# Kernel tuning notes

Hardware: AMD Instinct MI355X
Metric: run time of the kernel (lower is better)

Reference implementation:

```python
import jax, jax.numpy as jnp
import numpy as np

N = 100000      # nodes
E = 1600000     # edges
B = 64          # graphs in batch
V = 10000       # input_dim (embedding vocab)
EMB = 256       # emb_dim
HID = 64        # hidden_dim
OUT = 32        # output_dim


def setup_inputs() -> dict:
    key = jax.random.key(0)
    ks = jax.random.split(key, 12)
    state = jax.random.randint(ks[0], (B, 2), 0, V, dtype=jnp.int32)
    x = jax.random.randint(ks[1], (N,), 0, V, dtype=jnp.int32)
    edge_index = jax.random.randint(ks[2], (2, E), 0, N, dtype=jnp.int32)
    edge_weight = jnp.ones((E,), jnp.float32)
    # contiguous graph assignment (every graph non-empty)
    batch = jnp.minimum(jnp.arange(N, dtype=jnp.int32) // (N // B), B - 1)

    def lin(k, fin, fout):
        return jax.random.normal(k, (fin, fout), jnp.float32) / np.sqrt(fin).astype(np.float32)

    return {
        "state": state, "x": x, "edge_index": edge_index,
        "edge_weight": edge_weight, "batch": batch,
        "emb_table": jax.random.normal(ks[3], (V, EMB), jnp.float32),
        "W1": lin(ks[4], EMB, HID), "b1": jnp.zeros((HID,), jnp.float32),
        "W2": lin(ks[5], HID, HID), "b2": jnp.zeros((HID,), jnp.float32),
        "Wfc": lin(ks[6], HID, EMB), "bfc": jnp.zeros((EMB,), jnp.float32),
        "Wfc1": lin(ks[7], 3 * EMB, HID), "bfc1": jnp.zeros((HID,), jnp.float32),
        "Wfc2": lin(ks[8], HID, HID), "bfc2": jnp.zeros((HID,), jnp.float32),
        "Wfc3": lin(ks[9], HID, OUT), "bfc3": jnp.zeros((OUT,), jnp.float32),
    }


def gcn_conv(h, src, dst, ew, W, b):
    # PyG GCNConv: linear (no bias) -> sym-normalized aggregation w/ self loops -> + bias
    hw = h @ W                                           # [N, F_out]
    deg = jax.ops.segment_sum(ew, dst, num_segments=N) + 1.0  # +1 for self loop
    dinv = jax.lax.rsqrt(deg)                            # deg >= 1 always
    norm = dinv[src] * ew * dinv[dst]                    # [E]
    agg = jax.ops.segment_sum(norm[:, None] * hw[src], dst, num_segments=N)
    agg = agg + (dinv * dinv)[:, None] * hw              # self-loop contribution
    return agg + b


def reference(state, x, edge_index, edge_weight, batch, emb_table,
              W1, b1, W2, b2, Wfc, bfc, Wfc1, bfc1, Wfc2, bfc2, Wfc3, bfc3):
    src, dst = edge_index[0], edge_index[1]
    h = emb_table[x]                                     # [N, EMB]
    h = jax.nn.relu(gcn_conv(h, src, dst, edge_weight, W1, b1))
    h = gcn_conv(h, src, dst, edge_weight, W2, b2)       # [N, HID]
    # global mean pool over graphs
    counts = jax.ops.segment_sum(jnp.ones((N,), h.dtype), batch, num_segments=B)
    pooled = jax.ops.segment_sum(h, batch, num_segments=B) / jnp.maximum(counts, 1.0)[:, None]
    g = pooled @ Wfc + bfc                               # [B, EMB]
    x1 = emb_table[state[:, 0]]                          # [B, EMB]
    x2 = emb_table[state[:, 1]]                          # [B, EMB]
    z = jnp.concatenate([x1, x2, g], axis=-1)            # [B, 3*EMB]
    z = jax.nn.relu(z @ Wfc1 + bfc1)
    z = jax.nn.relu(z @ Wfc2 + bfc2)
    return z @ Wfc3 + bfc3                               # [B, OUT]
```

## Files before the change

kernel.cpp:

```cpp
#include <hip/hip_runtime.h>

#define NN   100000
#define NE   1600000
#define NB   64
#define NV   10000
#define EMB  256
#define HID  64
#define OUTD 32
#define NCH  ((NN + 1023) / 1024)

__device__ __forceinline__ void atomAddF(float* p, float v) {
  __hip_atomic_fetch_add(p, v, __ATOMIC_RELAXED, __HIP_MEMORY_SCOPE_AGENT);
}

__global__ void k_init_deg(float* deg, float* cntf, int n) {
  int i = blockIdx.x * blockDim.x + threadIdx.x;
  if (i < n) { deg[i] = 1.0f; cntf[i] = 0.0f; }
}

__global__ void k_deg_hist(const int* __restrict__ dst, const float* __restrict__ ew,
                           float* deg, int* cnt, int ne) {
  int e = blockIdx.x * blockDim.x + threadIdx.x;
  if (e < ne) {
    int d = dst[e];
    atomAddF(&deg[d], ew[e]);
    atomicAdd(&cnt[d], 1);
  }
}

__global__ void k_rsqrt(float* deg, int n) {
  int i = blockIdx.x * blockDim.x + threadIdx.x;
  if (i < n) deg[i] = rsqrtf(deg[i]);
}

__global__ __launch_bounds__(256) void k_blockred(const int* __restrict__ cnt, int* bsum, int n) {
  __shared__ int sh[256];
  int b = blockIdx.x, t = threadIdx.x;
  int base = b * 1024;
  int s = 0;
  for (int q = 0; q < 4; ++q) {
    int idx = base + q * 256 + t;
    if (idx < n) s += cnt[idx];
  }
  sh[t] = s; __syncthreads();
  for (int off = 128; off > 0; off >>= 1) {
    if (t < off) sh[t] += sh[t + off];
    __syncthreads();
  }
  if (t == 0) bsum[b] = sh[0];
}

__global__ void k_scan_small(int* bsum, int* rowptr, int nch, int n) {
  if (blockIdx.x == 0 && threadIdx.x == 0) {
    int run = 0;
    for (int i = 0; i < nch; ++i) { int t = bsum[i]; bsum[i] = run; run += t; }
    rowptr[n] = run;
  }
}

__global__ __launch_bounds__(256) void k_scan_chunk(const int* __restrict__ cnt,
                                                    const int* __restrict__ bsumx,
                                                    int* __restrict__ rowptr,
                                                    int* __restrict__ cursor, int n) {
  __shared__ int wsumS[4];
  int b = blockIdx.x, t = threadIdx.x, lane = t & 63, w = t >> 6;
  int base = b * 1024 + t * 4;
  int v0 = (base + 0 < n) ? cnt[base + 0] : 0;
  int v1 = (base + 1 < n) ? cnt[base + 1] : 0;
  int v2 = (base + 2 < n) ? cnt[base + 2] : 0;
  int v3 = (base + 3 < n) ? cnt[base + 3] : 0;
  int ts = v0 + v1 + v2 + v3;
  int x = ts;
  for (int d = 1; d < 64; d <<= 1) {
    int y = __shfl_up(x, d);
    if (lane >= d) x += y;
  }
  if (lane == 63) wsumS[w] = x;
  __syncthreads();
  int woff = 0;
  for (int q = 0; q < w; ++q) woff += wsumS[q];
  int excl = bsumx[b] + woff + x - ts;
  if (base + 0 < n) { rowptr[base + 0] = excl;              cursor[base + 0] = excl; }
  if (base + 1 < n) { rowptr[base + 1] = excl + v0;          cursor[base + 1] = excl + v0; }
  if (base + 2 < n) { rowptr[base + 2] = excl + v0 + v1;     cursor[base + 2] = excl + v0 + v1; }
  if (base + 3 < n) { rowptr[base + 3] = excl + v0 + v1 + v2; cursor[base + 3] = excl + v0 + v1 + v2; }
}

__global__ __launch_bounds__(256) void k_fill(const int* __restrict__ src,
                                              const int* __restrict__ dst,
                                              const float* __restrict__ ew,
                                              const float* __restrict__ dinv,
                                              int* cursor, int2* __restrict__ pad, int ne) {
  int e = blockIdx.x * blockDim.x + threadIdx.x;
  if (e < ne) {
    int s = src[e], d = dst[e];
    float nrm = dinv[s] * ew[e] * dinv[d];
    int pos = atomicAdd(&cursor[d], 1);
    pad[pos] = make_int2(s, __float_as_int(nrm));
  }
}

__global__ __launch_bounds__(256) void k_tab1(const float* __restrict__ emb,
                                              const float* __restrict__ W1,
                                              float* __restrict__ tab, int nv) {
  __shared__ float w1s[EMB * HID];
  int t = threadIdx.x;
  for (int i = t; i < EMB * HID; i += 256) w1s[i] = W1[i];
  __syncthreads();
  int lane = t & 63;
  int wid = __builtin_amdgcn_readfirstlane((blockIdx.x * 256 + t) >> 6);
  int nw = (gridDim.x * 256) >> 6;
  for (int i0 = wid * 4; i0 < nv; i0 += nw * 4) {
    const float* r0 = emb + (size_t)(i0 + 0) * EMB;
    const float* r1 = emb + (size_t)(i0 + 1) * EMB;
    const float* r2 = emb + (size_t)(i0 + 2) * EMB;
    const float* r3 = emb + (size_t)(i0 + 3) * EMB;
    float a0 = 0.f, a1 = 0.f, a2 = 0.f, a3 = 0.f;
#pragma unroll 8
    for (int k = 0; k < EMB; ++k) {
      float wv = w1s[k * HID + lane];
      a0 = fmaf(r0[k], wv, a0);
      a1 = fmaf(r1[k], wv, a1);
      a2 = fmaf(r2[k], wv, a2);
      a3 = fmaf(r3[k], wv, a3);
    }
    tab[(size_t)(i0 + 0) * HID + lane] = a0;
    tab[(size_t)(i0 + 1) * HID + lane] = a1;
    tab[(size_t)(i0 + 2) * HID + lane] = a2;
    tab[(size_t)(i0 + 3) * HID + lane] = a3;
  }
}

__global__ __launch_bounds__(256) void k_gemm2(const float* __restrict__ agg1,
                                               const float* __restrict__ W2,
                                               float* __restrict__ hw2, int n) {
  __shared__ float w2s[HID * HID];
  int t = threadIdx.x;
  for (int i = t; i < HID * HID; i += 256) w2s[i] = W2[i];
  __syncthreads();
  int lane = t & 63;
  int wid = __builtin_amdgcn_readfirstlane((blockIdx.x * 256 + t) >> 6);
  int nw = (gridDim.x * 256) >> 6;
  for (int i0 = wid * 4; i0 < n; i0 += nw * 4) {
    const float* r0 = agg1 + (size_t)(i0 + 0) * HID;
    const float* r1 = agg1 + (size_t)(i0 + 1) * HID;
    const float* r2 = agg1 + (size_t)(i0 + 2) * HID;
    const float* r3 = agg1 + (size_t)(i0 + 3) * HID;
    float a0 = 0.f, a1 = 0.f, a2 = 0.f, a3 = 0.f;
#pragma unroll 8
    for (int k = 0; k < HID; ++k) {
      float wv = w2s[k * HID + lane];
      a0 = fmaf(fmaxf(r0[k], 0.f), wv, a0);
      a1 = fmaf(fmaxf(r1[k], 0.f), wv, a1);
      a2 = fmaf(fmaxf(r2[k], 0.f), wv, a2);
      a3 = fmaf(fmaxf(r3[k], 0.f), wv, a3);
    }
    hw2[(size_t)(i0 + 0) * HID + lane] = a0;
    hw2[(size_t)(i0 + 1) * HID + lane] = a1;
    hw2[(size_t)(i0 + 2) * HID + lane] = a2;
    hw2[(size_t)(i0 + 3) * HID + lane] = a3;
  }
}

__global__ __launch_bounds__(256) void k_agg(const int* __restrict__ rowptr,
                                             const int2* __restrict__ pad,
                                             const float* __restrict__ H,
                                             const int* __restrict__ xmap,
                                             const float* __restrict__ dinv,
                                             const float* __restrict__ bias,
                                             float* __restrict__ aggout, int n) {
  int t = threadIdx.x;
  int lane = t & 63;
  int wid = __builtin_amdgcn_readfirstlane((blockIdx.x * 256 + t) >> 6);
  int nw = (gridDim.x * 256) >> 6;
  float bv = bias[lane];
  for (int d = wid; d < n; d += nw) {
    int r0 = __builtin_amdgcn_readfirstlane(rowptr[d]);
    int r1 = __builtin_amdgcn_readfirstlane(rowptr[d + 1]);
    float di = dinv[d];
    int srow = xmap ? xmap[d] : d;
    float acc = di * di * H[(size_t)srow * HID + lane] + bv;
    int j = r0;
    for (; j + 4 <= r1; j += 4) {
      int2 e0 = pad[j + 0];
      int2 e1 = pad[j + 1];
      int2 e2 = pad[j + 2];
      int2 e3 = pad[j + 3];
      int s0 = xmap ? xmap[e0.x] : e0.x;
      int s1 = xmap ? xmap[e1.x] : e1.x;
      int s2 = xmap ? xmap[e2.x] : e2.x;
      int s3 = xmap ? xmap[e3.x] : e3.x;
      acc = fmaf(__int_as_float(e0.y), H[(size_t)s0 * HID + lane], acc);
      acc = fmaf(__int_as_float(e1.y), H[(size_t)s1 * HID + lane], acc);
      acc = fmaf(__int_as_float(e2.y), H[(size_t)s2 * HID + lane], acc);
      acc = fmaf(__int_as_float(e3.y), H[(size_t)s3 * HID + lane], acc);
    }
    for (; j < r1; ++j) {
      int2 e = pad[j];
      int s = xmap ? xmap[e.x] : e.x;
      acc = fmaf(__int_as_float(e.y), H[(size_t)s * HID + lane], acc);
    }
    aggout[(size_t)d * HID + lane] = acc;
  }
}

__global__ void k_zero(float* p, int n) {
  int i = blockIdx.x * blockDim.x + threadIdx.x;
  if (i < n) p[i] = 0.f;
}

__global__ __launch_bounds__(256) void k_pool(const float* __restrict__ h,
                                              const int* __restrict__ batch,
                                              float* pooled, float* counts, int n) {
  int t = threadIdx.x;
  int lane = t & 63;
  int gw = (blockIdx.x * 256 + t) >> 6;
  int nw = (gridDim.x * 256) >> 6;
  int per = (n + nw - 1) / nw;
  int s = gw * per;
  int e = min(n, s + per);
  if (s >= e) return;
  int cur = batch[s];
  float acc = 0.f;
  int cnt = 0;
  for (int i = s; i < e; ++i) {
    int b = batch[i];
    if (b != cur) {
      atomAddF(&pooled[cur * HID + lane], acc);
      if (lane == 0) atomAddF(&counts[cur], (float)cnt);
      acc = 0.f; cnt = 0; cur = b;
    }
    acc += h[(size_t)i * HID + lane];
    cnt++;
  }
  atomAddF(&pooled[cur * HID + lane], acc);
  if (lane == 0) atomAddF(&counts[cur], (float)cnt);
}

__global__ __launch_bounds__(256) void k_head(const float* __restrict__ pooled,
                                              const float* __restrict__ counts,
                                              const float* __restrict__ emb,
                                              const int* __restrict__ state,
                                              const float* __restrict__ Wfc,  const float* __restrict__ bfc,
                                              const float* __restrict__ Wfc1, const float* __restrict__ bfc1,
                                              const float* __restrict__ Wfc2, const float* __restrict__ bfc2,
                                              const float* __restrict__ Wfc3, const float* __restrict__ bfc3,
                                              float* __restrict__ out) {
  __shared__ float z[3 * EMB];
  __shared__ float pm[HID];
  __shared__ float h1[HID];
  __shared__ float h2[HID];
  int b = blockIdx.x, t = threadIdx.x;
  if (t < HID) pm[t] = pooled[b * HID + t] / fmaxf(counts[b], 1.0f);
  __syncthreads();
  int s0 = state[2 * b], s1 = state[2 * b + 1];
  z[t]       = emb[(size_t)s0 * EMB + t];
  z[EMB + t] = emb[(size_t)s1 * EMB + t];
  float acc = bfc[t];
  for (int j = 0; j < HID; ++j) acc += pm[j] * Wfc[j * EMB + t];
  z[2 * EMB + t] = acc;
  __syncthreads();
  if (t < HID) {
    float a = bfc1[t];
    for (int k = 0; k < 3 * EMB; ++k) a += z[k] * Wfc1[k * HID + t];
    h1[t] = fmaxf(a, 0.f);
  }
  __syncthreads();
  if (t < HID) {
    float a = bfc2[t];
    for (int k = 0; k < HID; ++k) a += h1[k] * Wfc2[k * HID + t];
    h2[t] = fmaxf(a, 0.f);
  }
  __syncthreads();
  if (t < OUTD) {
    float a = bfc3[t];
    for (int k = 0; k < HID; ++k) a += h2[k] * Wfc3[k * OUTD + t];
    out[b * OUTD + t] = a;
  }
}

extern "C" void kernel_launch(void* const* d_in, const int* in_sizes, int n_in,
                              void* d_out, int out_size, void* d_ws, size_t ws_size,
                              hipStream_t stream) {
  const int*   state = (const int*)d_in[0];
  const int*   x     = (const int*)d_in[1];
  const int*   eidx  = (const int*)d_in[2];
  const int*   src   = eidx;
  const int*   dst   = eidx + NE;
  const float* ew    = (const float*)d_in[3];
  const int*   batch = (const int*)d_in[4];
  const float* emb   = (const float*)d_in[5];
  const float* W1    = (const float*)d_in[6];
  const float* b1    = (const float*)d_in[7];
  const float* W2    = (const float*)d_in[8];
  const float* b2    = (const float*)d_in[9];
  const float* Wfc   = (const float*)d_in[10];
  const float* bfc   = (const float*)d_in[11];
  const float* Wfc1  = (const float*)d_in[12];
  const float* bfc1  = (const float*)d_in[13];
  const float* Wfc2  = (const float*)d_in[14];
  const float* bfc2  = (const float*)d_in[15];
  const float* Wfc3  = (const float*)d_in[16];
  const float* bfc3  = (const float*)d_in[17];
  float* out = (float*)d_out;

  char* p = (char*)d_ws;
  auto alloc = [&](size_t bytes) -> void* {
    void* r = (void*)p;
    p += (bytes + 255) & ~(size_t)255;
    return r;
  };
  float* dinv   = (float*)alloc(NN * 4);
  int*   cnt    = (int*)  alloc(NN * 4);
  int*   rowptr = (int*)  alloc((NN + 1) * 4);
  int*   cursor = (int*)  alloc(NN * 4);
  int*   bsum   = (int*)  alloc(NCH * 4);
  int2*  pad    = (int2*) alloc((size_t)NE * 8);
  float* tab1   = (float*)alloc((size_t)NV * HID * 4);
  float* bufA   = (float*)alloc((size_t)NN * HID * 4);
  float* bufB   = (float*)alloc((size_t)NN * HID * 4);
  float* pooled = (float*)alloc(NB * HID * 4);
  float* counts = (float*)alloc(NB * 4);

  dim3 b256(256);
  int gN  = (NN + 255) / 256;
  int gE  = (NE + 255) / 256;

  k_init_deg<<<gN, b256, 0, stream>>>(dinv, (float*)cnt, NN);
  k_deg_hist<<<gE, b256, 0, stream>>>(dst, ew, dinv, cnt, NE);
  k_rsqrt<<<gN, b256, 0, stream>>>(dinv, NN);

  k_blockred<<<NCH, b256, 0, stream>>>(cnt, bsum, NN);
  k_scan_small<<<1, 64, 0, stream>>>(bsum, rowptr, NCH, NN);
  k_scan_chunk<<<NCH, b256, 0, stream>>>(cnt, bsum, rowptr, cursor, NN);

  k_fill<<<gE, b256, 0, stream>>>(src, dst, ew, dinv, cursor, pad, NE);

  k_tab1<<<625, b256, 0, stream>>>(emb, W1, tab1, NV);

  k_agg<<<2048, b256, 0, stream>>>(rowptr, pad, tab1, x, dinv, b1, bufB, NN);

  k_gemm2<<<1024, b256, 0, stream>>>(bufB, W2, bufA, NN);
  k_agg<<<2048, b256, 0, stream>>>(rowptr, pad, bufA, (const int*)nullptr, dinv, b2, bufB, NN);

  k_zero<<<(NB * HID + NB + 255) / 256, b256, 0, stream>>>(pooled, NB * HID + NB);
  k_pool<<<128, b256, 0, stream>>>(bufB, batch, pooled, counts, NN);

  k_head<<<NB, b256, 0, stream>>>(pooled, counts, emb, state,
                                  Wfc, bfc, Wfc1, bfc1, Wfc2, bfc2, Wfc3, bfc3, out);
}
```

Measured before the change: 652.8 us.

## Compute degree from CSR rows instead of float atomics, normalize in place

Removes the float atomic degree histogram and the separate init/rsqrt kernels. Edge weights are now stored raw in the CSR fill, then a per-node pass sums each row to get dinv and a second per-node pass rewrites the weights to normalized values. This trades E float atomics for two extra thread-per-node passes over the padded edge array, whose loops are uncoalesced and diverge with varying row lengths.

```diff
diff --git a/kernel.cpp b/kernel.cpp
--- a/kernel.cpp
+++ b/kernel.cpp
@@ -13,24 +13,9 @@
   __hip_atomic_fetch_add(p, v, __ATOMIC_RELAXED, __HIP_MEMORY_SCOPE_AGENT);
 }
 
-__global__ void k_init_deg(float* deg, float* cntf, int n) {
-  int i = blockIdx.x * blockDim.x + threadIdx.x;
-  if (i < n) { deg[i] = 1.0f; cntf[i] = 0.0f; }
-}
-
-__global__ void k_deg_hist(const int* __restrict__ dst, const float* __restrict__ ew,
-                           float* deg, int* cnt, int ne) {
+__global__ void k_cnt_hist(const int* __restrict__ dst, int* cnt, int ne) {
   int e = blockIdx.x * blockDim.x + threadIdx.x;
-  if (e < ne) {
-    int d = dst[e];
-    atomAddF(&deg[d], ew[e]);
-    atomicAdd(&cnt[d], 1);
-  }
-}
-
-__global__ void k_rsqrt(float* deg, int n) {
-  int i = blockIdx.x * blockDim.x + threadIdx.x;
-  if (i < n) deg[i] = rsqrtf(deg[i]);
+  if (e < ne) atomicAdd(&cnt[dst[e]], 1);
 }
 
 __global__ __launch_bounds__(256) void k_blockred(const int* __restrict__ cnt, int* bsum, int n) {
@@ -89,14 +74,37 @@
 __global__ __launch_bounds__(256) void k_fill(const int* __restrict__ src,
                                               const int* __restrict__ dst,
                                               const float* __restrict__ ew,
-                                              const float* __restrict__ dinv,
                                               int* cursor, int2* __restrict__ pad, int ne) {
   int e = blockIdx.x * blockDim.x + threadIdx.x;
   if (e < ne) {
-    int s = src[e], d = dst[e];
-    float nrm = dinv[s] * ew[e] * dinv[d];
-    int pos = atomicAdd(&cursor[d], 1);
-    pad[pos] = make_int2(s, __float_as_int(nrm));
+    int pos = atomicAdd(&cursor[dst[e]], 1);
+    pad[pos] = make_int2(src[e], __float_as_int(ew[e]));
+  }
+}
+
+__global__ __launch_bounds__(256) void k_deg(const int* __restrict__ rowptr,
+                                             const int2* __restrict__ pad,
+                                             float* __restrict__ dinv, int n) {
+  int i = blockIdx.x * blockDim.x + threadIdx.x;
+  if (i < n) {
+    int r0 = rowptr[i], r1 = rowptr[i + 1];
+    float s = 1.0f;
+    for (int j = r0; j < r1; ++j) s += __int_as_float(pad[j].y);
+    dinv[i] = rsqrtf(s);
+  }
+}
+
+__global__ __launch_bounds__(256) void k_norm(const int* __restrict__ rowptr,
+                                              const float* __restrict__ dinv,
+                                              int2* __restrict__ pad, int n) {
+  int i = blockIdx.x * blockDim.x + threadIdx.x;
+  if (i < n) {
+    int r0 = rowptr[i], r1 = rowptr[i + 1];
+    float dd = dinv[i];
+    for (int j = r0; j < r1; ++j) {
+      int2 e = pad[j];
+      pad[j].y = __float_as_int(dinv[e.x] * __int_as_float(e.y) * dd);
+    }
   }
 }
 
@@ -326,15 +334,15 @@
   int gN  = (NN + 255) / 256;
   int gE  = (NE + 255) / 256;
 
-  k_init_deg<<<gN, b256, 0, stream>>>(dinv, (float*)cnt, NN);
-  k_deg_hist<<<gE, b256, 0, stream>>>(dst, ew, dinv, cnt, NE);
-  k_rsqrt<<<gN, b256, 0, stream>>>(dinv, NN);
-
+  k_zero<<<gN, b256, 0, stream>>>((float*)cnt, NN);
+  k_cnt_hist<<<gE, b256, 0, stream>>>(dst, cnt, NE);
   k_blockred<<<NCH, b256, 0, stream>>>(cnt, bsum, NN);
   k_scan_small<<<1, 64, 0, stream>>>(bsum, rowptr, NCH, NN);
   k_scan_chunk<<<NCH, b256, 0, stream>>>(cnt, bsum, rowptr, cursor, NN);
-
-  k_fill<<<gE, b256, 0, stream>>>(src, dst, ew, dinv, cursor, pad, NE);
+  k_fill<<<gE, b256, 0, stream>>>(src, dst, ew, cursor, pad, NE);
+
+  k_deg<<<gN, b256, 0, stream>>>(rowptr, pad, dinv, NN);
+  k_norm<<<gN, b256, 0, stream>>>(rowptr, dinv, pad, NN);
 
   k_tab1<<<625, b256, 0, stream>>>(emb, W1, tab1, NV);
 
```

New measurement: 647.2 us. About the same (-0.8%).
